# Performance work log

Hardware: AMD Instinct MI355X
Metric: run time of the kernel (lower is better)

The kernel has to match this reference:

```python
import jax, jax.numpy as jnp
import numpy as np

B, L, D = 16, 2048, 128
GROUP = 16
NG = L // GROUP  # number of groups per batch
ALPHA = 0.5


def setup_inputs() -> dict:
    key = jax.random.key(0)
    k0, k1, k2 = jax.random.split(key, 3)
    x = jax.random.normal(k0, (B, L, D), dtype=jnp.float32)
    # per-batch permutation = gather indices (each position used exactly once)
    group_tensor = jax.vmap(lambda k: jax.random.permutation(k, L))(
        jax.random.split(k1, B)).astype(jnp.int32)
    ctxlens = jnp.full((B,), L, dtype=jnp.int32)
    W = jax.random.normal(k2, (2 * D,), dtype=jnp.float32) * (1.0 / np.sqrt(D))
    norm_alpha = jnp.ones((2,), dtype=jnp.float32)
    norm_gamma = jnp.ones((2 * D,), dtype=jnp.float32)
    norm_beta = jnp.zeros((2 * D,), dtype=jnp.float32)
    return {"x": x, "group_tensor": group_tensor, "ctxlens": ctxlens, "W": W,
            "norm_alpha": norm_alpha, "norm_gamma": norm_gamma, "norm_beta": norm_beta}


def _leaky_relu(v):
    return jnp.where(v >= 0, v, 0.01 * v)


def _ncn_forward(x, group_tensor, ctxlens, W, norm_alpha, norm_gamma, norm_beta):
    Bd, Ld, Dd = x.shape
    ng = Ld // GROUP
    Wi, Wj = W[:Dd], W[Dd:]
    a1, a2 = norm_alpha[0], norm_alpha[1]
    g1, g2 = norm_gamma[:Dd], norm_gamma[Dd:]
    b1, b2 = norm_beta[:Dd], norm_beta[Dd:]

    # gather x by group indices -> [B, NG, GROUP, D]
    xg = jnp.take_along_axis(x, group_tensor[:, :, None].astype(jnp.int32), axis=1)
    xg = xg.reshape(Bd, ng, GROUP, Dd)

    def step(carry, j):
        xi, xa = carry  # each [B, NG, GROUP, D]
        xj = jax.lax.dynamic_slice_in_dim(xi, j, 1, axis=2)  # [B, NG, 1, D]
        sim = jnp.einsum('bgnd,d->bgn', xi, Wi) \
            + jnp.einsum('bgd,d->bg', xj[:, :, 0, :], Wj)[:, :, None]  # [B,NG,GROUP]
        T = ALPHA * xi + (1.0 - ALPHA) * sim[..., None] * xj
        T_norm = g1 * jnp.tanh(a1 * T) + b1
        Fv = _leaky_relu(T_norm)
        xa = xa + Fv                               # ya = xa + F
        xi = xi + g2 * jnp.tanh(a2 * xa) + b2      # yi = xi + norm2(ya)
        return (xi, xa), None

    (yi, ya), _ = jax.lax.scan(step, (xg, jnp.zeros_like(xg)), jnp.arange(GROUP))

    # kernel only processes/stores a group if its start offset < ctxlen
    valid = (jnp.arange(ng, dtype=jnp.int32) * GROUP)[None, :] < ctxlens[:, None]
    yi = jnp.where(valid[:, :, None, None], yi, 0.0).reshape(Bd, Ld, Dd)
    ya = jnp.where(valid[:, :, None, None], ya, 0.0).reshape(Bd, Ld, Dd)

    # scatter back to original positions
    bidx = jnp.arange(Bd)[:, None]
    yi_out = jnp.zeros_like(x).at[bidx, group_tensor].set(yi)
    ya_out = jnp.zeros_like(x).at[bidx, group_tensor].set(ya)
    return yi_out, ya_out


def reference(x, group_tensor, ctxlens, W, norm_alpha, norm_gamma, norm_beta):
    return _ncn_forward(x, group_tensor, ctxlens, W, norm_alpha, norm_gamma, norm_beta)
```

## Files before the change

kernel.cpp:

```cpp
#include <hip/hip_runtime.h>

#define B_ 16
#define L_ 2048
#define D_ 128
#define GROUP_ 16
#define NG_ (L_ / GROUP_)

__global__ __launch_bounds__(256, 4) void ncn_kernel(
    const float* __restrict__ x,
    const int*   __restrict__ gt,
    const int*   __restrict__ ctxlens,
    const float* __restrict__ W,
    const float* __restrict__ nalpha,
    const float* __restrict__ ngamma,
    const float* __restrict__ nbeta,
    float* __restrict__ out)
{
    const int blk = blockIdx.x;
    const int b   = blk >> 7;
    const int g   = blk & (NG_ - 1);
    const int tid = threadIdx.x;
    const int row = tid >> 4;
    const int rl  = tid & 15;
    const int d0  = rl << 3;

    __shared__ float s_xj[2][D_];

    const float a1 = nalpha[0];
    const float a2 = nalpha[1];
    const float m1 = -2.0f * a1;
    const float m2 = -2.0f * a2;

    float Wi[8], Wj[8], G1[8], B1[8], G2[8], B2[8];
    {
        float g1r[8], b1r[8], g2r[8], b2r[8];
        *(float4*)&Wi[0]  = *(const float4*)(W + d0);
        *(float4*)&Wi[4]  = *(const float4*)(W + d0 + 4);
        *(float4*)&Wj[0]  = *(const float4*)(W + D_ + d0);
        *(float4*)&Wj[4]  = *(const float4*)(W + D_ + d0 + 4);
        *(float4*)&g1r[0] = *(const float4*)(ngamma + d0);
        *(float4*)&g1r[4] = *(const float4*)(ngamma + d0 + 4);
        *(float4*)&g2r[0] = *(const float4*)(ngamma + D_ + d0);
        *(float4*)&g2r[4] = *(const float4*)(ngamma + D_ + d0 + 4);
        *(float4*)&b1r[0] = *(const float4*)(nbeta + d0);
        *(float4*)&b1r[4] = *(const float4*)(nbeta + d0 + 4);
        *(float4*)&b2r[0] = *(const float4*)(nbeta + D_ + d0);
        *(float4*)&b2r[4] = *(const float4*)(nbeta + D_ + d0 + 4);
#pragma unroll
        for (int k = 0; k < 8; ++k) {
            G1[k] = 2.0f * g1r[k];
            B1[k] = b1r[k] - g1r[k];
            G2[k] = 2.0f * g2r[k];
            B2[k] = b2r[k] - g2r[k];
        }
    }
#pragma unroll
    for (int k = 0; k < 8; ++k) {
        asm volatile("" : "+v"(Wi[k]));
        asm volatile("" : "+v"(Wj[k]));
        asm volatile("" : "+v"(G1[k]));
        asm volatile("" : "+v"(B1[k]));
        asm volatile("" : "+v"(G2[k]));
        asm volatile("" : "+v"(B2[k]));
    }

    const int l   = g * GROUP_ + row;
    const int tok = gt[b * L_ + l];
    const float* xp = x + ((size_t)(b * L_ + tok)) * D_ + d0;

    float xi[8], xa[8];
    *(float4*)&xi[0] = *(const float4*)xp;
    *(float4*)&xi[4] = *(const float4*)(xp + 4);
#pragma unroll
    for (int k = 0; k < 8; ++k) xa[k] = 0.0f;

    if (row == 0) {
        *(float4*)&s_xj[0][d0]     = *(float4*)&xi[0];
        *(float4*)&s_xj[0][d0 + 4] = *(float4*)&xi[4];
    }
    __syncthreads();

    for (int j = 0; j < GROUP_; ++j) {
        const int p = j & 1;

        float xjv[8];
        *(float4*)&xjv[0] = *(const float4*)&s_xj[p][d0];
        *(float4*)&xjv[4] = *(const float4*)&s_xj[p][d0 + 4];

        float s = 0.0f;
#pragma unroll
        for (int k = 0; k < 8; ++k) s = fmaf(xi[k], Wi[k], s);
#pragma unroll
        for (int k = 0; k < 8; ++k) s = fmaf(xjv[k], Wj[k], s);
        s += __shfl_xor(s, 1);
        s += __shfl_xor(s, 2);
        s += __shfl_xor(s, 4);
        s += __shfl_xor(s, 8);
        const float s2 = 0.5f * s;

#pragma unroll
        for (int k = 0; k < 8; ++k) {
            float T  = fmaf(0.5f, xi[k], s2 * xjv[k]);
            float e1 = __expf(m1 * T);
            float r1 = __builtin_amdgcn_rcpf(1.0f + e1);
            float tn = fmaf(G1[k], r1, B1[k]);
            float Fv = fmaxf(tn, 0.01f * tn);
            xa[k] += Fv;
            float e2 = __expf(m2 * xa[k]);
            float r2 = __builtin_amdgcn_rcpf(1.0f + e2);
            xi[k] += fmaf(G2[k], r2, B2[k]);
        }

        if (j + 1 < GROUP_ && row == j + 1) {
            *(float4*)&s_xj[p ^ 1][d0]     = *(float4*)&xi[0];
            *(float4*)&s_xj[p ^ 1][d0 + 4] = *(float4*)&xi[4];
        }
        __syncthreads();
    }

    const bool valid = (g * GROUP_) < ctxlens[b];
    if (!valid) {
#pragma unroll
        for (int k = 0; k < 8; ++k) { xi[k] = 0.0f; xa[k] = 0.0f; }
    }

    float* o1 = out + ((size_t)(b * L_ + tok)) * D_ + d0;
    float* o2 = o1 + (size_t)B_ * L_ * D_;
    *(float4*)o1       = *(float4*)&xi[0];
    *(float4*)(o1 + 4) = *(float4*)&xi[4];
    *(float4*)o2       = *(float4*)&xa[0];
    *(float4*)(o2 + 4) = *(float4*)&xa[4];
}

extern "C" void kernel_launch(void* const* d_in, const int* in_sizes, int n_in,
                              void* d_out, int out_size, void* d_ws, size_t ws_size,
                              hipStream_t stream) {
    const float* x  = (const float*)d_in[0];
    const int*   gt = (const int*)d_in[1];
    const int*   cl = (const int*)d_in[2];
    const float* W  = (const float*)d_in[3];
    const float* na = (const float*)d_in[4];
    const float* ng = (const float*)d_in[5];
    const float* nb = (const float*)d_in[6];
    float* out = (float*)d_out;

    ncn_kernel<<<B_ * NG_, 256, 0, stream>>>(x, gt, cl, W, na, ng, nb, out);
}
```

Baseline: 123.5 us.

## Rescale recurrence to cut transcendental work and replace shuffles with DPP reductions

Folds the exponent scale factors into the gamma and beta constants and tracks the accumulator in scaled space, so each step uses exp2 directly. Batches eight reciprocals into one rcp plus multiplies via a prefix-product trick. Replaces the shuffle reduction with DPP row adds, and has the producer row precompute xj·Wj so the other rows skip that dot product. The exponent clamping and the batched reciprocal can change precision slightly and could overflow when the product of the eight denominators gets large.

```diff
diff --git a/kernel.cpp b/kernel.cpp
--- a/kernel.cpp
+++ b/kernel.cpp
@@ -5,6 +5,31 @@
 #define D_ 128
 #define GROUP_ 16
 #define NG_ (L_ / GROUP_)
+#define LOG2E_ 1.44269504088896340736f
+
+template<int CTRL>
+__device__ __forceinline__ float dpp_add(float v) {
+    int x = __builtin_amdgcn_update_dpp(0, __float_as_int(v), CTRL, 0xF, 0xF, false);
+    return v + __int_as_float(x);
+}
+__device__ __forceinline__ float row16_sum(float v) {
+    v = dpp_add<0xB1>(v);
+    v = dpp_add<0x4E>(v);
+    v = dpp_add<0x141>(v);
+    v = dpp_add<0x140>(v);
+    return v;
+}
+
+__device__ __forceinline__ void rcp8(const float d[8], float r[8]) {
+    float p[8];
+    p[0] = d[0];
+#pragma unroll
+    for (int k = 1; k < 8; ++k) p[k] = p[k - 1] * d[k];
+    float R = __builtin_amdgcn_rcpf(p[7]);
+#pragma unroll
+    for (int k = 7; k >= 1; --k) { r[k] = p[k - 1] * R; R *= d[k]; }
+    r[0] = R;
+}
 
 __global__ __launch_bounds__(256, 4) void ncn_kernel(
     const float* __restrict__ x,
@@ -25,13 +50,15 @@
     const int d0  = rl << 3;
 
     __shared__ float s_xj[2][D_];
+    __shared__ float s_sjW[2];
 
     const float a1 = nalpha[0];
     const float a2 = nalpha[1];
-    const float m1 = -2.0f * a1;
-    const float m2 = -2.0f * a2;
+    const float ca = -a1 * LOG2E_;
+    const float S  = -2.0f * a2 * LOG2E_;
+    const bool  selMin = (S < 0.0f);
 
-    float Wi[8], Wj[8], G1[8], B1[8], G2[8], B2[8];
+    float Wi[8], Wj[8], G1S[8], B1S[8], G2[8], B2[8];
     {
         float g1r[8], b1r[8], g2r[8], b2r[8];
         *(float4*)&Wi[0]  = *(const float4*)(W + d0);
@@ -48,18 +75,18 @@
         *(float4*)&b2r[4] = *(const float4*)(nbeta + D_ + d0 + 4);
 #pragma unroll
         for (int k = 0; k < 8; ++k) {
-            G1[k] = 2.0f * g1r[k];
-            B1[k] = b1r[k] - g1r[k];
-            G2[k] = 2.0f * g2r[k];
-            B2[k] = b2r[k] - g2r[k];
+            G1S[k] = S * 2.0f * g1r[k];
+            B1S[k] = S * (b1r[k] - g1r[k]);
+            G2[k]  = 2.0f * g2r[k];
+            B2[k]  = b2r[k] - g2r[k];
         }
     }
 #pragma unroll
     for (int k = 0; k < 8; ++k) {
         asm volatile("" : "+v"(Wi[k]));
         asm volatile("" : "+v"(Wj[k]));
-        asm volatile("" : "+v"(G1[k]));
-        asm volatile("" : "+v"(B1[k]));
+        asm volatile("" : "+v"(G1S[k]));
+        asm volatile("" : "+v"(B1S[k]));
         asm volatile("" : "+v"(G2[k]));
         asm volatile("" : "+v"(B2[k]));
     }
@@ -68,55 +95,77 @@
     const int tok = gt[b * L_ + l];
     const float* xp = x + ((size_t)(b * L_ + tok)) * D_ + d0;
 
-    float xi[8], xa[8];
+    float xi[8], za[8];
     *(float4*)&xi[0] = *(const float4*)xp;
     *(float4*)&xi[4] = *(const float4*)(xp + 4);
 #pragma unroll
-    for (int k = 0; k < 8; ++k) xa[k] = 0.0f;
+    for (int k = 0; k < 8; ++k) za[k] = 0.0f;
 
     if (row == 0) {
         *(float4*)&s_xj[0][d0]     = *(float4*)&xi[0];
         *(float4*)&s_xj[0][d0 + 4] = *(float4*)&xi[4];
+        float w = 0.0f;
+#pragma unroll
+        for (int k = 0; k < 8; ++k) w = fmaf(xi[k], Wj[k], w);
+        w = row16_sum(w);
+        if (rl == 0) s_sjW[0] = w;
     }
-    __syncthreads();
 
     for (int j = 0; j < GROUP_; ++j) {
+        __syncthreads();
         const int p = j & 1;
 
         float xjv[8];
         *(float4*)&xjv[0] = *(const float4*)&s_xj[p][d0];
         *(float4*)&xjv[4] = *(const float4*)&s_xj[p][d0 + 4];
+        const float sjW = s_sjW[p];
 
         float s = 0.0f;
 #pragma unroll
         for (int k = 0; k < 8; ++k) s = fmaf(xi[k], Wi[k], s);
+        s = row16_sum(s);
+        const float sim = s + sjW;
+        const float cb  = ca * sim;
+
+        float darr[8], r1[8];
 #pragma unroll
-        for (int k = 0; k < 8; ++k) s = fmaf(xjv[k], Wj[k], s);
-        s += __shfl_xor(s, 1);
-        s += __shfl_xor(s, 2);
-        s += __shfl_xor(s, 4);
-        s += __shfl_xor(s, 8);
-        const float s2 = 0.5f * s;
+        for (int k = 0; k < 8; ++k) {
+            float u = fmaf(ca, xi[k], cb * xjv[k]);
+            u = fminf(u, 15.0f);
+            darr[k] = 1.0f + __builtin_amdgcn_exp2f(u);
+        }
+        rcp8(darr, r1);
 
 #pragma unroll
         for (int k = 0; k < 8; ++k) {
-            float T  = fmaf(0.5f, xi[k], s2 * xjv[k]);
-            float e1 = __expf(m1 * T);
-            float r1 = __builtin_amdgcn_rcpf(1.0f + e1);
-            float tn = fmaf(G1[k], r1, B1[k]);
-            float Fv = fmaxf(tn, 0.01f * tn);
-            xa[k] += Fv;
-            float e2 = __expf(m2 * xa[k]);
-            float r2 = __builtin_amdgcn_rcpf(1.0f + e2);
-            xi[k] += fmaf(G2[k], r2, B2[k]);
+            float tnS = fmaf(G1S[k], r1[k], B1S[k]);
+            float alt = 0.01f * tnS;
+            float FvS = selMin ? fminf(tnS, alt) : fmaxf(tnS, alt);
+            za[k] += FvS;
+            float z = fminf(za[k], 15.0f);
+            darr[k] = 1.0f + __builtin_amdgcn_exp2f(z);
         }
+        rcp8(darr, r1);
 
-        if (j + 1 < GROUP_ && row == j + 1) {
+#pragma unroll
+        for (int k = 0; k < 8; ++k)
+            xi[k] += fmaf(G2[k], r1[k], B2[k]);
+
+        if (row == j + 1) {
             *(float4*)&s_xj[p ^ 1][d0]     = *(float4*)&xi[0];
             *(float4*)&s_xj[p ^ 1][d0 + 4] = *(float4*)&xi[4];
+            float w = 0.0f;
+#pragma unroll
+            for (int k = 0; k < 8; ++k) w = fmaf(xi[k], Wj[k], w);
+            w = row16_sum(w);
+            if (rl == 0) s_sjW[p ^ 1] = w;
         }
-        __syncthreads();
     }
+
+    const float invS = 1.0f / S;
+    float xa[8];
+#pragma unroll
+    for (int k = 0; k < 8; ++k) xa[k] = za[k] * invS;
 
     const bool valid = (g * GROUP_) < ctxlens[b];
     if (!valid) {
```

Measured after the change: 122.6 us. Within noise of the previous version (-0.7%).
